# Optimization experiments

Measured on AMD Instinct MI355X. Metric: run time of the kernel, lower is better.

Reference implementation:

```python
import jax, jax.numpy as jnp
import numpy as np
import math

NUM_HEADS = 8

def setup_inputs() -> dict:
    key = jax.random.key(0)
    ks = jax.random.split(key, 20)
    N, n, M, E = 4096, 3, 16, 256
    nE = 65536
    s = lambda k, shape: (jax.random.normal(k, shape, jnp.float32) * 0.02)
    return {
        "equ": jax.random.normal(ks[0], (N, n, M), jnp.float32),
        "h": jax.random.normal(ks[1], (N, E), jnp.float32),
        "edge_index": jax.random.randint(ks[2], (2, nE), 0, N),
        "edge_fea": jax.random.normal(ks[3], (nE, 4), jnp.float32),
        "W_equ": s(ks[4], (M, E)),
        "W_gproj": s(ks[5], (E, 32)),
        "W_vg": s(ks[6], (E, E)),
        "W_g1": s(ks[7], (32 * 32, 2 * E)), "b_g1": jnp.zeros((2 * E,), jnp.float32),
        "W_g2": s(ks[8], (2 * E, E)), "b_g2": jnp.zeros((E,), jnp.float32),
        "W_q": s(ks[9], (2 * E, E)), "b_q": jnp.zeros((E,), jnp.float32),
        "W_k": s(ks[10], (2 * E, E)), "b_k": jnp.zeros((E,), jnp.float32),
        "W_v": s(ks[11], (2 * E, E)), "b_v": jnp.zeros((E,), jnp.float32),
        "W_ng": s(ks[12], (E, E)), "b_ng": jnp.zeros((E,), jnp.float32),
        "W_gout": s(ks[13], (E, E)),
        "W_gdec": s(ks[14], (E, M)),
        "W_hdec": s(ks[15], (E, E)), "b_hdec": jnp.zeros((E,), jnp.float32),
    }


def reference(equ, h, edge_index, edge_fea, W_equ, W_gproj, W_vg, W_g1, b_g1,
              W_g2, b_g2, W_q, b_q, W_k, b_k, W_v, b_v, W_ng, b_ng,
              W_gout, W_gdec, W_hdec, b_hdec):
    # edge_index / edge_fea are unused in the original forward (dead args).
    N, n, M = equ.shape
    E = W_equ.shape[1]
    H = NUM_HEADS
    D = E // H
    scaling = D ** -0.5
    sqrtE = math.sqrt(E)

    g_src = (equ @ W_equ) * sqrtE                     # [N, n, E]
    h_src = h * sqrtE                                 # [N, E]

    g2 = g_src @ W_gproj                              # [N, n, 32]
    gram = jnp.einsum('nia,nib->nab', g2, g2)         # [N, 32, 32]
    g2 = gram.reshape(N, 32 * 32)
    g2 = jax.nn.relu(g2 @ W_g1 + b_g1) @ W_g2 + b_g2  # [N, E]

    h2 = jnp.concatenate([g2, h_src], axis=-1)        # [N, 2E]
    q = ((h2 @ W_q + b_q) * scaling).reshape(N, H, D)
    k = (h2 @ W_k + b_k).reshape(N, H, D)
    v = (h2 @ W_v + b_v).reshape(N, H, D)
    vg = (g_src @ W_vg).reshape(N, n, H, D)           # [N, n, H, D]

    attn = jax.nn.softmax(jnp.einsum('nhd,mhd->hnm', q, k), axis=-1)  # [H, N, N]

    out_v = jnp.einsum('hnm,mhd->nhd', attn, v).reshape(N, E)
    h_src1 = out_v @ W_ng + b_ng                      # [N, E]

    # Same attention probs reused for the vector channel (torch does repeat+bmm;
    # we broadcast instead of materializing the repeated [n*H, N, N] tensor).
    out_g = jnp.einsum('hnm,mvhd->nvhd', attn, vg).reshape(N, n, E)
    g_src1 = out_g @ W_gout                           # [N, n, E]

    g_src = g_src + g_src1
    h_src = h_src + h_src1
    equ_out = g_src @ W_gdec                          # [N, n, M]
    h_out = h_src @ W_hdec + b_hdec                   # [N, E]
    return (equ_out, h_out)
```

## Files before the change

kernel.cpp:

```cpp
#include <hip/hip_runtime.h>
#include <hip/hip_bf16.h>

typedef __attribute__((ext_vector_type(8))) short short8;
typedef __attribute__((ext_vector_type(4))) float floatx4;

constexpr int N_ = 4096;
constexpr float SQRT_E = 16.0f;
constexpr float QSCALE = 0.17677669529663687f * 1.4426950408889634f;

__device__ __forceinline__ ushort f2bf(float x) {
  __hip_bfloat16 h = __float2bfloat16(x);
  return *reinterpret_cast<ushort*>(&h);
}
__device__ __forceinline__ float bf2f(ushort b) {
  unsigned int u = ((unsigned int)b) << 16;
  return __uint_as_float(u);
}

__device__ __forceinline__ float dpp_max16(float x) {
  int v = __float_as_int(x);
  int y;
  y = __builtin_amdgcn_update_dpp(v, v, 0x128, 0xf, 0xf, false);
  v = __float_as_int(fmaxf(__int_as_float(v), __int_as_float(y)));
  y = __builtin_amdgcn_update_dpp(v, v, 0x124, 0xf, 0xf, false);
  v = __float_as_int(fmaxf(__int_as_float(v), __int_as_float(y)));
  y = __builtin_amdgcn_update_dpp(v, v, 0x122, 0xf, 0xf, false);
  v = __float_as_int(fmaxf(__int_as_float(v), __int_as_float(y)));
  y = __builtin_amdgcn_update_dpp(v, v, 0x121, 0xf, 0xf, false);
  v = __float_as_int(fmaxf(__int_as_float(v), __int_as_float(y)));
  return __int_as_float(v);
}

__device__ __forceinline__ void do_transpose(
    const float* __restrict__ src, ushort* __restrict__ dsth,
    ushort* __restrict__ dstl, int R, int C, int lb, int cb_shift,
    float* smem, int hasLo)
{
  float (*tile)[33] = (float(*)[33])smem;
  const int r0 = (lb >> cb_shift) * 32;
  const int c0 = (lb & ((1 << cb_shift) - 1)) * 32;
  const int tx = threadIdx.x & 31, ty = threadIdx.x >> 5;
  #pragma unroll
  for (int p = 0; p < 4; ++p) {
    const int lr = p*8 + ty;
    tile[lr][tx] = (r0+lr < R && c0+tx < C) ? src[(size_t)(r0+lr)*C + c0 + tx] : 0.f;
  }
  __syncthreads();
  #pragma unroll
  for (int p = 0; p < 4; ++p) {
    const int dc = p*8 + ty;
    if (c0+dc < C && r0+tx < R) {
      const float v = tile[tx][dc];
      const ushort hi = f2bf(v);
      dsth[(size_t)(c0+dc)*R + r0 + tx] = hi;
      if (hasLo) dstl[(size_t)(c0+dc)*R + r0 + tx] = f2bf(v - bf2f(hi));
    }
  }
}

__global__ __launch_bounds__(256) void k_prep(
    const float* __restrict__ equ, const float* __restrict__ h,
    const float* __restrict__ W_equ, const float* __restrict__ W_gproj,
    const float* __restrict__ W_g1, const float* __restrict__ W_g2,
    const float* __restrict__ W_q, const float* __restrict__ W_k,
    const float* __restrict__ W_v, const float* __restrict__ W_vg,
    const float* __restrict__ W_ng, const float* __restrict__ W_gout,
    const float* __restrict__ W_hdec, const float* __restrict__ W_gdec,
    ushort* __restrict__ Wg1t, ushort* __restrict__ Wg2t,
    ushort* __restrict__ Wth, ushort* __restrict__ Wtl,
    ushort* __restrict__ Wvgt, ushort* __restrict__ Wngt,
    ushort* __restrict__ Wgoutt, ushort* __restrict__ Whdect,
    ushort* __restrict__ Wgdect,
    ushort* __restrict__ h2h, ushort* __restrict__ h2l,
    ushort* __restrict__ vt,
    ushort* __restrict__ g_src_b, ushort* __restrict__ gram_b)
{
  __shared__ __align__(16) float smem[1056];
  const int b = blockIdx.x;
  const int t = threadIdx.x;

  if (b < 512) {
    do_transpose(W_g1, Wg1t, nullptr, 1024, 512, b, 4, smem, 0);
  } else if (b < 640) {
    do_transpose(W_g2, Wg2t, nullptr, 512, 256, b-512, 3, smem, 0);
  } else if (b < 768) {
    do_transpose(W_q, Wth, Wtl, 512, 256, b-640, 3, smem, 1);
  } else if (b < 896) {
    do_transpose(W_k, Wth + 256*512, Wtl + 256*512, 512, 256, b-768, 3, smem, 1);
  } else if (b < 1024) {
    do_transpose(W_v, Wth + 512*512, Wtl + 512*512, 512, 256, b-896, 3, smem, 1);
  } else if (b < 1088) {
    do_transpose(W_vg, Wvgt, nullptr, 256, 256, b-1024, 3, smem, 0);
  } else if (b < 1152) {
    do_transpose(W_ng, Wngt, nullptr, 256, 256, b-1088, 3, smem, 0);
  } else if (b < 1216) {
    do_transpose(W_gout, Wgoutt, nullptr, 256, 256, b-1152, 3, smem, 0);
  } else if (b < 1280) {
    do_transpose(W_hdec, Whdect, nullptr, 256, 256, b-1216, 3, smem, 0);
  } else if (b < 1288) {
    do_transpose(W_gdec, Wgdect, nullptr, 256, 16, b-1280, 0, smem, 0);
  } else if (b < 5384) {
    const int i = b - 1288;
    const float v = h[(size_t)i*256 + t] * SQRT_E;
    const ushort hi = f2bf(v);
    h2h[(size_t)i*512 + 256 + t] = hi;
    h2l[(size_t)i*512 + 256 + t] = f2bf(v - bf2f(hi));
  } else if (b < 7432) {
    const int idx = (b - 5384)*256 + t;
    const int n = idx & 4095;
    const int c16 = (idx >> 12) & 15;
    const int hh = idx >> 16;
    vt[((size_t)hh*144 + 128 + c16)*N_ + n] = (c16 == 0) ? (ushort)0x3F80 : (ushort)0;
  } else {
    float* eq  = smem;
    float* gs  = smem + 48;
    float* g2p = smem + 816;
    const int i = b - 7432;
    if (t < 48) eq[t] = equ[(size_t)i*48 + t];
    __syncthreads();
    #pragma unroll
    for (int j = 0; j < 3; ++j) {
      float s = 0.f;
      #pragma unroll
      for (int m = 0; m < 16; ++m) s += eq[j*16+m] * W_equ[m*256 + t];
      s *= SQRT_E;
      gs[j*256 + t] = s;
      g_src_b[((size_t)i*3 + j)*256 + t] = f2bf(s);
    }
    __syncthreads();
    if (t < 96) {
      const int j = t >> 5, a = t & 31;
      float s = 0.f;
      for (int e = 0; e < 256; ++e) s += gs[j*256+e] * W_gproj[e*32 + a];
      g2p[t] = s;
    }
    __syncthreads();
    #pragma unroll
    for (int r = 0; r < 4; ++r) {
      const int idx = r*256 + t;
      const int a = idx >> 5, bb = idx & 31;
      const float s = g2p[a]*g2p[bb] + g2p[32+a]*g2p[32+bb] + g2p[64+a]*g2p[64+bb];
      gram_b[(size_t)i*1024 + idx] = f2bf(s);
    }
  }
}

template<int KTOT>
__device__ __forceinline__ void gemm_core(
    const ushort* __restrict__ A, const ushort* __restrict__ Bt,
    int bM, int bN, floatx4 acc[4], ushort* As, ushort* Bs)
{
  const int t = threadIdx.x;
  const int wave = t >> 6, lane = t & 63, quad = lane >> 4, m = lane & 15;
  #pragma unroll
  for (int ct = 0; ct < 4; ++ct) acc[ct] = {0.f, 0.f, 0.f, 0.f};
  const int ca = t*2, cb = t*2 + 1;
  const int ra = ca >> 3, pa = ca & 7;
  const int rb = cb >> 3, pb = cb & 7;
  const ushort* pA0 = A  + (size_t)(bM+ra)*KTOT + pa*8;
  const ushort* pA1 = A  + (size_t)(bM+rb)*KTOT + pb*8;
  const ushort* pB0 = Bt + (size_t)(bN+ra)*KTOT + pa*8;
  const ushort* pB1 = Bt + (size_t)(bN+rb)*KTOT + pb*8;
  short8 rA0 = *(const short8*)pA0, rA1 = *(const short8*)pA1;
  short8 rB0 = *(const short8*)pB0, rB1 = *(const short8*)pB1;
  for (int k0 = 0; k0 < KTOT; k0 += 64) {
    __syncthreads();
    *(short8*)&As[ra*72 + pa*8] = rA0;
    *(short8*)&As[rb*72 + pb*8] = rA1;
    *(short8*)&Bs[ra*72 + pa*8] = rB0;
    *(short8*)&Bs[rb*72 + pb*8] = rB1;
    if (k0 + 64 < KTOT) {
      pA0 += 64; pA1 += 64; pB0 += 64; pB1 += 64;
      rA0 = *(const short8*)pA0; rA1 = *(const short8*)pA1;
      rB0 = *(const short8*)pB0; rB1 = *(const short8*)pB1;
    }
    __syncthreads();
    #pragma unroll
    for (int ks = 0; ks < 2; ++ks) {
      const short8 af = *(const short8*)&As[(wave*16 + m)*72 + ks*32 + quad*8];
      #pragma unroll
      for (int ct = 0; ct < 4; ++ct) {
        const short8 bf = *(const short8*)&Bs[(ct*16 + m)*72 + ks*32 + quad*8];
        acc[ct] = __builtin_amdgcn_mfma_f32_16x16x32_bf16(af, bf, acc[ct], 0, 0, 0);
      }
    }
  }
}

template<int KTOT>
__device__ __forceinline__ void gemm_core3(
    const ushort* __restrict__ Ah, const ushort* __restrict__ Al,
    const ushort* __restrict__ Bth, const ushort* __restrict__ Btl,
    int bM, int bN, floatx4 acc[4],
    ushort* Ash, ushort* Asl, ushort* Bsh, ushort* Bsl)
{
  const int t = threadIdx.x;
  const int wave = t >> 6, lane = t & 63, quad = lane >> 4, m = lane & 15;
  #pragma unroll
  for (int ct = 0; ct < 4; ++ct) acc[ct] = {0.f, 0.f, 0.f, 0.f};
  const int ca = t*2, cb = t*2 + 1;
  const int ra = ca >> 3, pa = ca & 7;
  const int rb = cb >> 3, pb = cb & 7;
  const ushort* pAh0 = Ah  + (size_t)(bM+ra)*KTOT + pa*8;
  const ushort* pAh1 = Ah  + (size_t)(bM+rb)*KTOT + pb*8;
  const ushort* pAl0 = Al  + (size_t)(bM+ra)*KTOT + pa*8;
  const ushort* pAl1 = Al  + (size_t)(bM+rb)*KTOT + pb*8;
  const ushort* pBh0 = Bth + (size_t)(bN+ra)*KTOT + pa*8;
  const ushort* pBh1 = Bth + (size_t)(bN+rb)*KTOT + pb*8;
  const ushort* pBl0 = Btl + (size_t)(bN+ra)*KTOT + pa*8;
  const ushort* pBl1 = Btl + (size_t)(bN+rb)*KTOT + pb*8;
  short8 rAh0 = *(const short8*)pAh0, rAh1 = *(const short8*)pAh1;
  short8 rAl0 = *(const short8*)pAl0, rAl1 = *(const short8*)pAl1;
  short8 rBh0 = *(const short8*)pBh0, rBh1 = *(const short8*)pBh1;
  short8 rBl0 = *(const short8*)pBl0, rBl1 = *(const short8*)pBl1;
  for (int k0 = 0; k0 < KTOT; k0 += 64) {
    __syncthreads();
    *(short8*)&Ash[ra*72 + pa*8] = rAh0;
    *(short8*)&Ash[rb*72 + pb*8] = rAh1;
    *(short8*)&Asl[ra*72 + pa*8] = rAl0;
    *(short8*)&Asl[rb*72 + pb*8] = rAl1;
    *(short8*)&Bsh[ra*72 + pa*8] = rBh0;
    *(short8*)&Bsh[rb*72 + pb*8] = rBh1;
    *(short8*)&Bsl[ra*72 + pa*8] = rBl0;
    *(short8*)&Bsl[rb*72 + pb*8] = rBl1;
    if (k0 + 64 < KTOT) {
      pAh0 += 64; pAh1 += 64; pAl0 += 64; pAl1 += 64;
      pBh0 += 64; pBh1 += 64; pBl0 += 64; pBl1 += 64;
      rAh0 = *(const short8*)pAh0; rAh1 = *(const short8*)pAh1;
      rAl0 = *(const short8*)pAl0; rAl1 = *(const short8*)pAl1;
      rBh0 = *(const short8*)pBh0; rBh1 = *(const short8*)pBh1;
      rBl0 = *(const short8*)pBl0; rBl1 = *(const short8*)pBl1;
    }
    __syncthreads();
    #pragma unroll
    for (int ks = 0; ks < 2; ++ks) {
      const short8 ah = *(const short8*)&Ash[(wave*16 + m)*72 + ks*32 + quad*8];
      const short8 al = *(const short8*)&Asl[(wave*16 + m)*72 + ks*32 + quad*8];
      #pragma unroll
      for (int ct = 0; ct < 4; ++ct) {
        const short8 bh = *(const short8*)&Bsh[(ct*16 + m)*72 + ks*32 + quad*8];
        const short8 bl = *(const short8*)&Bsl[(ct*16 + m)*72 + ks*32 + quad*8];
        acc[ct] = __builtin_amdgcn_mfma_f32_16x16x32_bf16(ah, bl, acc[ct], 0, 0, 0);
        acc[ct] = __builtin_amdgcn_mfma_f32_16x16x32_bf16(al, bh, acc[ct], 0, 0, 0);
        acc[ct] = __builtin_amdgcn_mfma_f32_16x16x32_bf16(ah, bh, acc[ct], 0, 0, 0);
      }
    }
  }
}

__global__ __launch_bounds__(256) void k_g1(
    const ushort* __restrict__ gram_b, const ushort* __restrict__ Wg1t,
    const float* __restrict__ b_g1, ushort* __restrict__ hidden)
{
  __shared__ __align__(16) ushort As[64*72], Bs[64*72];
  floatx4 acc[4];
  const int bM = blockIdx.x*64, bN = blockIdx.y*64;
  gemm_core<1024>(gram_b, Wg1t, bM, bN, acc, As, Bs);
  const int lane = threadIdx.x & 63, wave = threadIdx.x >> 6;
  const int quad = lane >> 4, m = lane & 15;
  #pragma unroll
  for (int ct = 0; ct < 4; ++ct) {
    const int c = bN + ct*16 + m;
    #pragma unroll
    for (int r = 0; r < 4; ++r) {
      const int i = bM + wave*16 + quad*4 + r;
      hidden[(size_t)i*512 + c] = f2bf(fmaxf(acc[ct][r] + b_g1[c], 0.f));
    }
  }
}

__global__ __launch_bounds__(256) void k_g2(
    const ushort* __restrict__ hidden, const ushort* __restrict__ Wg2t,
    const float* __restrict__ b_g2, ushort* __restrict__ h2h, ushort* __restrict__ h2l)
{
  __shared__ __align__(16) ushort As[64*72], Bs[64*72];
  floatx4 acc[4];
  const int bM = blockIdx.x*64, bN = blockIdx.y*64;
  gemm_core<512>(hidden, Wg2t, bM, bN, acc, As, Bs);
  const int lane = threadIdx.x & 63, wave = threadIdx.x >> 6;
  const int quad = lane >> 4, m = lane & 15;
  #pragma unroll
  for (int ct = 0; ct < 4; ++ct) {
    const int c = bN + ct*16 + m;
    #pragma unroll
    for (int r = 0; r < 4; ++r) {
      const int i = bM + wave*16 + quad*4 + r;
      const float s = acc[ct][r] + b_g2[c];
      const ushort hi = f2bf(s);
      h2h[(size_t)i*512 + c] = hi;
      h2l[(size_t)i*512 + c] = f2bf(s - bf2f(hi));
    }
  }
}

__global__ __launch_bounds__(256) void k_g34(
    const ushort* __restrict__ h2h, const ushort* __restrict__ h2l,
    const ushort* __restrict__ Wth, const ushort* __restrict__ Wtl,
    const float* __restrict__ b_q, const float* __restrict__ b_k,
    const float* __restrict__ b_v,
    const ushort* __restrict__ g_src_b, const ushort* __restrict__ Wvgt,
    float* __restrict__ q_ws, ushort* __restrict__ kh, ushort* __restrict__ kl,
    ushort* __restrict__ vt)
{
  __shared__ __align__(16) ushort S0[64*72], S1[64*72], S2[64*72], S3[64*72];
  const int lb = blockIdx.y*192 + blockIdx.x;
  const int lane = threadIdx.x & 63, wave = threadIdx.x >> 6;
  const int quad = lane >> 4, m = lane & 15;
  floatx4 acc[4];
  if (lb < 768) {
    const int bM = (lb & 63)*64, bN = (lb >> 6)*64;
    if (bN < 512) {
      gemm_core3<512>(h2h, h2l, Wth, Wtl, bM, bN, acc, S0, S1, S2, S3);
      #pragma unroll
      for (int ct = 0; ct < 4; ++ct) {
        const int c = bN + ct*16 + m;
        #pragma unroll
        for (int r = 0; r < 4; ++r) {
          const int i = bM + wave*16 + quad*4 + r;
          if (c < 256) {
            const float s = acc[ct][r] + b_q[c];
            q_ws[((size_t)(c >> 5)*N_ + i)*32 + (c & 31)] = s * QSCALE;
          } else {
            const int cc = c - 256;
            const float s = acc[ct][r] + b_k[cc];
            const ushort hi = f2bf(s);
            kh[((size_t)(cc >> 5)*N_ + i)*32 + (cc & 31)] = hi;
            kl[((size_t)(cc >> 5)*N_ + i)*32 + (cc & 31)] = f2bf(s - bf2f(hi));
          }
        }
      }
    } else {
      gemm_core<512>(h2h, Wth, bM, bN, acc, S0, S1);
      #pragma unroll
      for (int ct = 0; ct < 4; ++ct) {
        const int cc = bN + ct*16 + m - 512;
        #pragma unroll
        for (int r = 0; r < 4; ++r) {
          const int i = bM + wave*16 + quad*4 + r;
          const float s = acc[ct][r] + b_v[cc];
          vt[((size_t)(cc >> 5)*144 + (cc & 31))*N_ + i] = f2bf(s);
        }
      }
    }
  } else {
    const int lb2 = lb - 768;
    const int bM = (lb2 >> 2)*64, bN = (lb2 & 3)*64;
    gemm_core<256>(g_src_b, Wvgt, bM, bN, acc, S0, S1);
    #pragma unroll
    for (int ct = 0; ct < 4; ++ct) {
      const int c = bN + ct*16 + m;
      const int hh = c >> 5, d = c & 31;
      #pragma unroll
      for (int r = 0; r < 4; ++r) {
        const int i3 = bM + wave*16 + quad*4 + r;
        const int i = i3 / 3, j = i3 - 3*i;
        vt[((size_t)hh*144 + 32 + j*32 + d)*N_ + i] = f2bf(acc[ct][r]);
      }
    }
  }
}

__global__ __launch_bounds__(256, 4) void k3_attn(
    const float* __restrict__ q_ws, const ushort* __restrict__ kh,
    const ushort* __restrict__ kl, const ushort* __restrict__ vt,
    ushort* __restrict__ Po0, ushort* __restrict__ Po1, ushort* __restrict__ Po2,
    float* __restrict__ Pml)
{
  __shared__ __align__(16) ushort Khs[64*40], Kls[64*40];
  __shared__ __align__(16) ushort Vs[144*64];
  __shared__ __align__(16) ushort Pl[4*16*72];
  __shared__ float li_s[64];

  const int t    = threadIdx.x;
  const int wave = t >> 6;
  const int lane = t & 63;
  const int quad = lane >> 4;
  const int m    = lane & 15;
  const int h    = blockIdx.y;
  const int s    = blockIdx.z;
  const int n0q  = blockIdx.x * 64;

  const int ktb = (s == 0) ? 0  : (s == 1 ? 22 : 43);
  const int kte = (s == 0) ? 22 : (s == 1 ? 43 : 64);

  union { short8 v; ushort u[8]; } Aqh, Aql;
  {
    const float* qp = q_ws + ((size_t)h*N_ + n0q + wave*16 + m)*32 + quad*8;
    #pragma unroll
    for (int jj = 0; jj < 8; ++jj) {
      const float x = qp[jj];
      const ushort hi = f2bf(x);
      Aqh.u[jj] = hi;
      Aql.u[jj] = f2bf(x - bf2f(hi));
    }
  }

  floatx4 Of[9];
  #pragma unroll
  for (int nt = 0; nt < 9; ++nt) Of[nt] = {0.f, 0.f, 0.f, 0.f};
  float mi[4];
  #pragma unroll
  for (int r = 0; r < 4; ++r) mi[r] = -3.0e38f;

  const int krow = t >> 2, kch = (t & 3) * 8;

  const ushort* pKh = kh + ((size_t)h*N_ + ktb*64 + krow)*32 + kch;
  const ushort* pKl = kl + ((size_t)h*N_ + ktb*64 + krow)*32 + kch;
  const ushort* pV[4];
  int wV[4];
  #pragma unroll
  for (int p = 0; p < 4; ++p) {
    const int idx = p*256 + t, row = idx >> 3, g = idx & 7;
    pV[p] = vt + ((size_t)h*144 + row)*N_ + ktb*64 + g*8;
    wV[p] = (row*8 + (g ^ (row & 7)))*8;
  }
  const ushort* pV4 = nullptr;
  int wV4 = 0;
  if (t < 128) {
    const int idx = 1024 + t, row = idx >> 3, g = idx & 7;
    pV4 = vt + ((size_t)h*144 + row)*N_ + ktb*64 + g*8;
    wV4 = (row*8 + (g ^ (row & 7)))*8;
  }

  short8 rK0 = *(const short8*)pKh;
  short8 rK1 = *(const short8*)pKl;
  short8 rV[4], rV4e;
  #pragma unroll
  for (int p = 0; p < 4; ++p) rV[p] = *(const short8*)pV[p];
  if (t < 128) rV4e = *(const short8*)pV4;

  for (int kt = ktb; kt < kte; ++kt) {
    __syncthreads();
    *(short8*)&Khs[krow*40 + kch] = rK0;
    *(short8*)&Kls[krow*40 + kch] = rK1;
    #pragma unroll
    for (int p = 0; p < 4; ++p) *(short8*)&Vs[wV[p]] = rV[p];
    if (t < 128) *(short8*)&Vs[wV4] = rV4e;
    if (kt + 1 < kte) {
      pKh += 2048; pKl += 2048;
      rK0 = *(const short8*)pKh;
      rK1 = *(const short8*)pKl;
      #pragma unroll
      for (int p = 0; p < 4; ++p) { pV[p] += 64; rV[p] = *(const short8*)pV[p]; }
      if (t < 128) { pV4 += 64; rV4e = *(const short8*)pV4; }
    }
    __syncthreads();

    floatx4 sf[4];
    #pragma unroll
    for (int kb = 0; kb < 4; ++kb) {
      const short8 bkh = *(const short8*)&Khs[(kb*16 + m)*40 + quad*8];
      const short8 bkl = *(const short8*)&Kls[(kb*16 + m)*40 + quad*8];
      floatx4 sv = {0.f, 0.f, 0.f, 0.f};
      sv = __builtin_amdgcn_mfma_f32_16x16x32_bf16(Aqh.v, bkl, sv, 0, 0, 0);
      sv = __builtin_amdgcn_mfma_f32_16x16x32_bf16(Aql.v, bkh, sv, 0, 0, 0);
      sv = __builtin_amdgcn_mfma_f32_16x16x32_bf16(Aqh.v, bkh, sv, 0, 0, 0);
      sf[kb] = sv;
    }

    float tm[4];
    bool need = false;
    #pragma unroll
    for (int r = 0; r < 4; ++r) {
      float nm = fmaxf(fmaxf(sf[0][r], sf[1][r]), fmaxf(sf[2][r], sf[3][r]));
      tm[r] = dpp_max16(nm);
      need |= (tm[r] > mi[r] + 20.f);
    }
    if (__any(need)) {
      #pragma unroll
      for (int r = 0; r < 4; ++r) {
        const float mn = fmaxf(mi[r], tm[r]);
        const float al = exp2f(mi[r] - mn);
        mi[r] = mn;
        #pragma unroll
        for (int nt = 0; nt < 9; ++nt) Of[nt][r] *= al;
      }
    }
    #pragma unroll
    for (int kb = 0; kb < 4; ++kb)
      #pragma unroll
      for (int r = 0; r < 4; ++r) {
        const float pv = exp2f(sf[kb][r] - mi[r]);
        Pl[wave*1152 + (quad*4 + r)*72 + kb*16 + m] =
            (ushort)(__float_as_uint(pv) >> 16);
      }

    #pragma unroll
    for (int ks = 0; ks < 2; ++ks) {
      const short8 ap = *(const short8*)&Pl[wave*1152 + m*72 + ks*32 + quad*8];
      #pragma unroll
      for (int nt = 0; nt < 9; ++nt) {
        const int row = nt*16 + m;
        const int pos = (ks*4 + quad) ^ (row & 7);
        const short8 bv = *(const short8*)&Vs[(row*8 + pos)*8];
        Of[nt] = __builtin_amdgcn_mfma_f32_16x16x32_bf16(ap, bv, Of[nt], 0, 0, 0);
      }
    }
  }

  if (m == 0) {
    #pragma unroll
    for (int r = 0; r < 4; ++r) li_s[wave*16 + quad*4 + r] = Of[8][r];
  }
  __syncthreads();
  const floatx4 liv = *(const floatx4*)&li_s[wave*16 + quad*4];
  float linv[4];
  #pragma unroll
  for (int r = 0; r < 4; ++r) linv[r] = 1.0f / liv[r];

  ushort* Po = (s == 0) ? Po0 : ((s == 1) ? Po1 : Po2);
  #pragma unroll
  for (int nt = 0; nt < 8; ++nt) {
    #pragma unroll
    for (int r = 0; r < 4; ++r) {
      const int n = n0q + wave*16 + quad*4 + r;
      Po[((size_t)h*N_ + n)*128 + nt*16 + m] = f2bf(Of[nt][r] * linv[r]);
    }
  }
  if (m == 0) {
    #pragma unroll
    for (int r = 0; r < 4; ++r) {
      const int n = n0q + wave*16 + quad*4 + r;
      Pml[(((size_t)s*8 + h)*N_ + n)*2 + 0] = mi[r];
      Pml[(((size_t)s*8 + h)*N_ + n)*2 + 1] = Of[8][r];
    }
  }
}

__global__ __launch_bounds__(256) void k_merge(
    const ushort* __restrict__ Po0, const ushort* __restrict__ Po1,
    const ushort* __restrict__ Po2, const float* __restrict__ Pml,
    ushort* __restrict__ out_v_b, ushort* __restrict__ out_g_b)
{
  const int idx = blockIdx.x*256 + threadIdx.x;
  const int c0 = (idx & 15) * 8;
  const int n  = (idx >> 4) & 4095;
  const int h  = idx >> 16;
  const float m1 = Pml[(((size_t)0*8 + h)*N_ + n)*2 + 0];
  const float l1 = Pml[(((size_t)0*8 + h)*N_ + n)*2 + 1];
  const float m2 = Pml[(((size_t)1*8 + h)*N_ + n)*2 + 0];
  const float l2 = Pml[(((size_t)1*8 + h)*N_ + n)*2 + 1];
  const float m3 = Pml[(((size_t)2*8 + h)*N_ + n)*2 + 0];
  const float l3 = Pml[(((size_t)2*8 + h)*N_ + n)*2 + 1];
  const float M = fmaxf(fmaxf(m1, m2), m3);
  const float w1 = exp2f(m1 - M) * l1;
  const float w2 = exp2f(m2 - M) * l2;
  const float w3 = exp2f(m3 - M) * l3;
  const float inv = 1.0f / (w1 + w2 + w3);
  union { short8 v; ushort u[8]; } a, b, c, res;
  a.v = *(const short8*)&Po0[((size_t)h*N_ + n)*128 + c0];
  b.v = *(const short8*)&Po1[((size_t)h*N_ + n)*128 + c0];
  c.v = *(const short8*)&Po2[((size_t)h*N_ + n)*128 + c0];
  #pragma unroll
  for (int j = 0; j < 8; ++j)
    res.u[j] = f2bf((w1*bf2f(a.u[j]) + w2*bf2f(b.u[j]) + w3*bf2f(c.u[j])) * inv);
  if (c0 < 32) {
    *(short8*)&out_v_b[(size_t)n*256 + h*32 + c0] = res.v;
  } else {
    const int j = (c0 - 32) >> 5, cc = (c0 - 32) & 31;
    *(short8*)&out_g_b[((size_t)n*3 + j)*256 + h*32 + cc] = res.v;
  }
}

__global__ __launch_bounds__(256) void k56ab(
    const ushort* __restrict__ out_v_b, const ushort* __restrict__ Wngt,
    const float* __restrict__ b_ng, const float* __restrict__ h,
    ushort* __restrict__ tmp_b,
    const ushort* __restrict__ out_g_b, const ushort* __restrict__ Wgoutt,
    const ushort* __restrict__ g_src_b, ushort* __restrict__ gsum_b)
{
  __shared__ __align__(16) ushort As[64*72], Bs[64*72];
  floatx4 acc[4];
  const int lane = threadIdx.x & 63, wave = threadIdx.x >> 6;
  const int quad = lane >> 4, m = lane & 15;
  const int bN = blockIdx.y*64;
  if (blockIdx.x < 64) {
    const int bM = blockIdx.x*64;
    gemm_core<256>(out_v_b, Wngt, bM, bN, acc, As, Bs);
    #pragma unroll
    for (int ct = 0; ct < 4; ++ct) {
      const int c = bN + ct*16 + m;
      #pragma unroll
      for (int r = 0; r < 4; ++r) {
        const int i = bM + wave*16 + quad*4 + r;
        tmp_b[(size_t)i*256 + c] =
            f2bf(acc[ct][r] + b_ng[c] + h[(size_t)i*256 + c] * SQRT_E);
      }
    }
  } else {
    const int bM = (blockIdx.x - 64)*64;
    gemm_core<256>(out_g_b, Wgoutt, bM, bN, acc, As, Bs);
    #pragma unroll
    for (int ct = 0; ct < 4; ++ct) {
      const int c = bN + ct*16 + m;
      #pragma unroll
      for (int r = 0; r < 4; ++r) {
        const int i = bM + wave*16 + quad*4 + r;
        gsum_b[(size_t)i*256 + c] =
            f2bf(acc[ct][r] + bf2f(g_src_b[(size_t)i*256 + c]));
      }
    }
  }
}

__global__ __launch_bounds__(256) void k56cd(
    const ushort* __restrict__ tmp_b, const ushort* __restrict__ Whdect,
    const float* __restrict__ b_hdec,
    const ushort* __restrict__ gsum_b, const ushort* __restrict__ Wgdect,
    float* __restrict__ out)
{
  __shared__ __align__(16) ushort As[64*72], Bs[64*72];
  const int t = threadIdx.x;
  const int lane = t & 63, wave = t >> 6;
  const int quad = lane >> 4, m = lane & 15;
  if (blockIdx.x < 64) {
    floatx4 acc[4];
    const int bM = blockIdx.x*64, bN = blockIdx.y*64;
    gemm_core<256>(tmp_b, Whdect, bM, bN, acc, As, Bs);
    #pragma unroll
    for (int ct = 0; ct < 4; ++ct) {
      const int c = bN + ct*16 + m;
      #pragma unroll
      for (int r = 0; r < 4; ++r) {
        const int i = bM + wave*16 + quad*4 + r;
        out[196608 + (size_t)i*256 + c] = acc[ct][r] + b_hdec[c];
      }
    }
  } else if (blockIdx.y == 0) {
    const int bM = (blockIdx.x - 64)*64;
    floatx4 acc = {0.f, 0.f, 0.f, 0.f};
    const int row = t >> 2, kq = (t & 3) * 8;
    for (int k0 = 0; k0 < 256; k0 += 32) {
      __syncthreads();
      *(short8*)&As[row*40 + kq] = *(const short8*)&gsum_b[(size_t)(bM+row)*256 + k0 + kq];
      if (t < 64)
        *(short8*)&Bs[(t>>2)*40 + kq] = *(const short8*)&Wgdect[(size_t)(t>>2)*256 + k0 + kq];
      __syncthreads();
      const short8 af = *(const short8*)&As[(wave*16 + m)*40 + quad*8];
      const short8 bf = *(const short8*)&Bs[m*40 + quad*8];
      acc = __builtin_amdgcn_mfma_f32_16x16x32_bf16(af, bf, acc, 0, 0, 0);
    }
    #pragma unroll
    for (int r = 0; r < 4; ++r)
      out[(size_t)(bM + wave*16 + quad*4 + r)*16 + m] = acc[r];
  }
}

extern "C" void kernel_launch(void* const* d_in, const int* in_sizes, int n_in,
                              void* d_out, int out_size, void* d_ws, size_t ws_size,
                              hipStream_t stream) {
  const float* equ    = (const float*)d_in[0];
  const float* h      = (const float*)d_in[1];
  const float* W_equ  = (const float*)d_in[4];
  const float* W_gproj= (const float*)d_in[5];
  const float* W_vg   = (const float*)d_in[6];
  const float* W_g1   = (const float*)d_in[7];
  const float* b_g1   = (const float*)d_in[8];
  const float* W_g2   = (const float*)d_in[9];
  const float* b_g2   = (const float*)d_in[10];
  const float* W_q    = (const float*)d_in[11];
  const float* b_q    = (const float*)d_in[12];
  const float* W_k    = (const float*)d_in[13];
  const float* b_k    = (const float*)d_in[14];
  const float* W_v    = (const float*)d_in[15];
  const float* b_v    = (const float*)d_in[16];
  const float* W_ng   = (const float*)d_in[17];
  const float* b_ng   = (const float*)d_in[18];
  const float* W_gout = (const float*)d_in[19];
  const float* W_gdec = (const float*)d_in[20];
  const float* W_hdec = (const float*)d_in[21];
  const float* b_hdec = (const float*)d_in[22];
  float* out = (float*)d_out;

  char* wsb = (char*)d_ws;
  constexpr size_t MiB = 1048576;
  float*  q_ws    = (float*) (wsb +  0*MiB);
  ushort* kh      = (ushort*)(wsb +  4*MiB);
  ushort* kl      = (ushort*)(wsb +  6*MiB);
  ushort* vt      = (ushort*)(wsb +  8*MiB);
  ushort* h2h     = (ushort*)(wsb + 17*MiB);
  ushort* h2l     = (ushort*)(wsb + 21*MiB);
  ushort* g_src_b = (ushort*)(wsb + 25*MiB);
  ushort* wbase   = (ushort*)(wsb + 31*MiB);
  ushort* Wg1t = wbase;
  ushort* Wg2t = wbase + 524288;
  ushort* Wth  = wbase + 655360;
  ushort* Wtl  = wbase + 1048576;
  ushort* Wvgt = wbase + 1441792;
  ushort* wbase2  = (ushort*)(wsb + 34*MiB);
  ushort* Wngt   = wbase2;
  ushort* Wgoutt = wbase2 + 65536;
  ushort* Whdect = wbase2 + 131072;
  ushort* Wgdect = wbase2 + 196608;
  ushort* gram_b  = (ushort*)(wsb + 34*MiB + 524288);
  ushort* hidden  = (ushort*)(wsb + 42*MiB + 524288);
  ushort* Po0     = (ushort*)(wsb + 17*MiB);
  ushort* Po1     = (ushort*)(wsb + 34*MiB + 524288);
  ushort* Po2     = (ushort*)(wsb + 42*MiB + 524288);
  float*  Pml     = (float*) (wsb + 50*MiB + 524288);
  ushort* out_v_b = (ushort*)(wsb +  4*MiB);
  ushort* out_g_b = (ushort*)(wsb +  8*MiB);
  ushort* tmp_b   = (ushort*)(wsb + 42*MiB + 524288);
  ushort* gsum_b  = (ushort*)(wsb + 34*MiB + 524288);

  k_prep<<<11528, 256, 0, stream>>>(
      equ, h, W_equ, W_gproj, W_g1, W_g2, W_q, W_k, W_v,
      W_vg, W_ng, W_gout, W_hdec, W_gdec,
      Wg1t, Wg2t, Wth, Wtl, Wvgt, Wngt, Wgoutt, Whdect, Wgdect,
      h2h, h2l, vt, g_src_b, gram_b);

  k_g1<<<dim3(64, 8), 256, 0, stream>>>(gram_b, Wg1t, b_g1, hidden);
  k_g2<<<dim3(64, 4), 256, 0, stream>>>(hidden, Wg2t, b_g2, h2h, h2l);
  k_g34<<<dim3(192, 8), 256, 0, stream>>>(h2h, h2l, Wth, Wtl, b_q, b_k, b_v,
                                          g_src_b, Wvgt, q_ws, kh, kl, vt);

  dim3 g3(64, 8, 3);
  k3_attn<<<g3, 256, 0, stream>>>(q_ws, kh, kl, vt, Po0, Po1, Po2, Pml);
  k_merge<<<2048, 256, 0, stream>>>(Po0, Po1, Po2, Pml, out_v_b, out_g_b);

  k56ab<<<dim3(256, 4), 256, 0, stream>>>(out_v_b, Wngt, b_ng, h, tmp_b,
                                          out_g_b, Wgoutt, g_src_b, gsum_b);
  k56cd<<<dim3(256, 4), 256, 0, stream>>>(tmp_b, Whdect, b_hdec,
                                          gsum_b, Wgdect, out);
}
```

Before: 299.7 us.

## Halve attention key tile to 32 and split gram projection across threads

The attention kernel now streams keys in 32-row tiles instead of 64, so LDS and prefetch registers shrink and the launch bound rises from 4 to 5 blocks per SIMD. The K/V tile loads are reassigned to match, and the V swizzle switches to 4 groups. The trade-off is twice as many loop iterations and barriers for the same work. Separately, the gram projection in the prep kernel splits its 256-long dot product over 192 threads in two halves and reduces them through shared memory.

```diff
diff --git a/kernel.cpp b/kernel.cpp
--- a/kernel.cpp
+++ b/kernel.cpp
@@ -75,7 +75,7 @@
     ushort* __restrict__ vt,
     ushort* __restrict__ g_src_b, ushort* __restrict__ gram_b)
 {
-  __shared__ __align__(16) float smem[1056];
+  __shared__ __align__(16) float smem[1120];
   const int b = blockIdx.x;
   const int t = threadIdx.x;
 
@@ -112,9 +112,10 @@
     const int hh = idx >> 16;
     vt[((size_t)hh*144 + 128 + c16)*N_ + n] = (c16 == 0) ? (ushort)0x3F80 : (ushort)0;
   } else {
-    float* eq  = smem;
-    float* gs  = smem + 48;
-    float* g2p = smem + 816;
+    float* eq   = smem;
+    float* gs   = smem + 48;
+    float* g2p  = smem + 816;
+    float* part = smem + 912;
     const int i = b - 7432;
     if (t < 48) eq[t] = equ[(size_t)i*48 + t];
     __syncthreads();
@@ -128,12 +129,17 @@
       g_src_b[((size_t)i*3 + j)*256 + t] = f2bf(s);
     }
     __syncthreads();
-    if (t < 96) {
-      const int j = t >> 5, a = t & 31;
+    if (t < 192) {
+      const int o = t % 96, half = t / 96;
+      const int j = o >> 5, a = o & 31;
+      const int e0 = half * 128;
       float s = 0.f;
-      for (int e = 0; e < 256; ++e) s += gs[j*256+e] * W_gproj[e*32 + a];
-      g2p[t] = s;
-    }
+      for (int e = 0; e < 128; ++e)
+        s += gs[j*256 + e0 + e] * W_gproj[(size_t)(e0+e)*32 + a];
+      part[t] = s;
+    }
+    __syncthreads();
+    if (t < 96) g2p[t] = part[t] + part[96 + t];
     __syncthreads();
     #pragma unroll
     for (int r = 0; r < 4; ++r) {
@@ -360,15 +366,15 @@
   }
 }
 
-__global__ __launch_bounds__(256, 4) void k3_attn(
+__global__ __launch_bounds__(256, 5) void k3_attn(
     const float* __restrict__ q_ws, const ushort* __restrict__ kh,
     const ushort* __restrict__ kl, const ushort* __restrict__ vt,
     ushort* __restrict__ Po0, ushort* __restrict__ Po1, ushort* __restrict__ Po2,
     float* __restrict__ Pml)
 {
-  __shared__ __align__(16) ushort Khs[64*40], Kls[64*40];
-  __shared__ __align__(16) ushort Vs[144*64];
-  __shared__ __align__(16) ushort Pl[4*16*72];
+  __shared__ __align__(16) ushort Khs[32*40], Kls[32*40];
+  __shared__ __align__(16) ushort Vs[144*32];
+  __shared__ __align__(16) ushort Pl[4*16*40];
   __shared__ float li_s[64];
 
   const int t    = threadIdx.x;
@@ -380,8 +386,8 @@
   const int s    = blockIdx.z;
   const int n0q  = blockIdx.x * 64;
 
-  const int ktb = (s == 0) ? 0  : (s == 1 ? 22 : 43);
-  const int kte = (s == 0) ? 22 : (s == 1 ? 43 : 64);
+  const int ktb = (s == 0) ? 0  : (s == 1 ? 43 : 86);
+  const int kte = (s == 0) ? 43 : (s == 1 ? 86 : 128);
 
   union { short8 v; ushort u[8]; } Aqh, Aql;
   {
@@ -402,53 +408,46 @@
   #pragma unroll
   for (int r = 0; r < 4; ++r) mi[r] = -3.0e38f;
 
-  const int krow = t >> 2, kch = (t & 3) * 8;
-
-  const ushort* pKh = kh + ((size_t)h*N_ + ktb*64 + krow)*32 + kch;
-  const ushort* pKl = kl + ((size_t)h*N_ + ktb*64 + krow)*32 + kch;
-  const ushort* pV[4];
-  int wV[4];
-  #pragma unroll
-  for (int p = 0; p < 4; ++p) {
-    const int idx = p*256 + t, row = idx >> 3, g = idx & 7;
-    pV[p] = vt + ((size_t)h*144 + row)*N_ + ktb*64 + g*8;
-    wV[p] = (row*8 + (g ^ (row & 7)))*8;
-  }
-  const ushort* pV4 = nullptr;
-  int wV4 = 0;
-  if (t < 128) {
-    const int idx = 1024 + t, row = idx >> 3, g = idx & 7;
-    pV4 = vt + ((size_t)h*144 + row)*N_ + ktb*64 + g*8;
-    wV4 = (row*8 + (g ^ (row & 7)))*8;
-  }
-
-  short8 rK0 = *(const short8*)pKh;
-  short8 rK1 = *(const short8*)pKl;
-  short8 rV[4], rV4e;
-  #pragma unroll
-  for (int p = 0; p < 4; ++p) rV[p] = *(const short8*)pV[p];
-  if (t < 128) rV4e = *(const short8*)pV4;
+  const int tt = t & 127;
+  const int krow = tt >> 2, kch = (tt & 3) * 8;
+  const ushort* pK = ((t < 128) ? kh : kl)
+                     + ((size_t)h*N_ + ktb*32 + krow)*32 + kch;
+  const int vrow0 = t >> 2,        vg0 = t & 3;
+  const int vrow1 = (256+t) >> 2,  vg1 = (256+t) & 3;
+  const int vrow2 = (512+t) >> 2,  vg2 = (512+t) & 3;
+  const ushort* pV0 = vt + ((size_t)h*144 + vrow0)*N_ + ktb*32 + vg0*8;
+  const ushort* pV1 = vt + ((size_t)h*144 + vrow1)*N_ + ktb*32 + vg1*8;
+  const ushort* pV2 = vt + ((size_t)h*144 + vrow2)*N_ + ktb*32 + vg2*8;
+  const int wV0 = (vrow0*4 + (vg0 ^ (vrow0 & 3)))*8;
+  const int wV1 = (vrow1*4 + (vg1 ^ (vrow1 & 3)))*8;
+  const int wV2 = (vrow2*4 + (vg2 ^ (vrow2 & 3)))*8;
+
+  short8 rK  = *(const short8*)pK;
+  short8 rV0 = *(const short8*)pV0;
+  short8 rV1 = *(const short8*)pV1;
+  short8 rV2e;
+  if (t < 64) rV2e = *(const short8*)pV2;
 
   for (int kt = ktb; kt < kte; ++kt) {
     __syncthreads();
-    *(short8*)&Khs[krow*40 + kch] = rK0;
-    *(short8*)&Kls[krow*40 + kch] = rK1;
-    #pragma unroll
-    for (int p = 0; p < 4; ++p) *(short8*)&Vs[wV[p]] = rV[p];
-    if (t < 128) *(short8*)&Vs[wV4] = rV4e;
+    if (t < 128) *(short8*)&Khs[krow*40 + kch] = rK;
+    else         *(short8*)&Kls[krow*40 + kch] = rK;
+    *(short8*)&Vs[wV0] = rV0;
+    *(short8*)&Vs[wV1] = rV1;
+    if (t < 64) *(short8*)&Vs[wV2] = rV2e;
     if (kt + 1 < kte) {
-      pKh += 2048; pKl += 2048;
-      rK0 = *(const short8*)pKh;
-      rK1 = *(const short8*)pKl;
-      #pragma unroll
-      for (int p = 0; p < 4; ++p) { pV[p] += 64; rV[p] = *(const short8*)pV[p]; }
-      if (t < 128) { pV4 += 64; rV4e = *(const short8*)pV4; }
-    }
-    __syncthreads();
-
-    floatx4 sf[4];
-    #pragma unroll
-    for (int kb = 0; kb < 4; ++kb) {
+      pK += 1024;
+      rK = *(const short8*)pK;
+      pV0 += 32; pV1 += 32;
+      rV0 = *(const short8*)pV0;
+      rV1 = *(const short8*)pV1;
+      if (t < 64) { pV2 += 32; rV2e = *(const short8*)pV2; }
+    }
+    __syncthreads();
+
+    floatx4 sf[2];
+    #pragma unroll
+    for (int kb = 0; kb < 2; ++kb) {
       const short8 bkh = *(const short8*)&Khs[(kb*16 + m)*40 + quad*8];
       const short8 bkl = *(const short8*)&Kls[(kb*16 + m)*40 + quad*8];
       floatx4 sv = {0.f, 0.f, 0.f, 0.f};
@@ -462,7 +461,7 @@
     bool need = false;
     #pragma unroll
     for (int r = 0; r < 4; ++r) {
-      float nm = fmaxf(fmaxf(sf[0][r], sf[1][r]), fmaxf(sf[2][r], sf[3][r]));
+      float nm = fmaxf(sf[0][r], sf[1][r]);
       tm[r] = dpp_max16(nm);
       need |= (tm[r] > mi[r] + 20.f);
     }
@@ -477,22 +476,21 @@
       }
     }
     #pragma unroll
-    for (int kb = 0; kb < 4; ++kb)
+    for (int kb = 0; kb < 2; ++kb)
       #pragma unroll
       for (int r = 0; r < 4; ++r) {
         const float pv = exp2f(sf[kb][r] - mi[r]);
-        Pl[wave*1152 + (quad*4 + r)*72 + kb*16 + m] =
+        Pl[wave*640 + (quad*4 + r)*40 + kb*16 + m] =
             (ushort)(__float_as_uint(pv) >> 16);
       }
 
-    #pragma unroll
-    for (int ks = 0; ks < 2; ++ks) {
-      const short8 ap = *(const short8*)&Pl[wave*1152 + m*72 + ks*32 + quad*8];
+    {
+      const short8 ap = *(const short8*)&Pl[wave*640 + m*40 + quad*8];
       #pragma unroll
       for (int nt = 0; nt < 9; ++nt) {
         const int row = nt*16 + m;
-        const int pos = (ks*4 + quad) ^ (row & 7);
-        const short8 bv = *(const short8*)&Vs[(row*8 + pos)*8];
+        const int pos = quad ^ (row & 3);
+        const short8 bv = *(const short8*)&Vs[(row*4 + pos)*8];
         Of[nt] = __builtin_amdgcn_mfma_f32_16x16x32_bf16(ap, bv, Of[nt], 0, 0, 0);
       }
     }
```

After: 331.2 us. +10.5%, slower.
